# Kernel optimization log

Measured on AMD Instinct MI355X. Metric: run time of the kernel, lower is better.

## Reference

```python
import jax, jax.numpy as jnp
import numpy as np

B, H, S, D = 512, 1024, 1024, 128
TOPK = 32

def setup_inputs() -> dict:
    key = jax.random.key(0)
    ks = jax.random.split(key, 12)
    w = lambda k, shape: (jax.random.normal(k, shape, dtype=jnp.float32) * 0.02)
    return {
        "latent": jax.random.normal(ks[0], (B, H), dtype=jnp.float32),
        "memory": jax.random.normal(ks[1], (B, S, D), dtype=jnp.float32),
        "read_query_w": w(ks[2], (H, D)),
        "read_query_b": jnp.zeros((D,), jnp.float32),
        "memory_key": w(ks[3], (S, D)),
        "write_gate_w": w(ks[4], (H + D, 1)),
        "write_gate_b": jnp.zeros((1,), jnp.float32),
        "dmd_proj_w": w(ks[5], (H + D, 1)),
        "dmd_proj_b": jnp.zeros((1,), jnp.float32),
        "phase_proj_w": w(ks[6], (H, 1)),
        "phase_proj_b": jnp.zeros((1,), jnp.float32),
        "write_value_w": w(ks[7], (H, D)),
        "write_value_b": jnp.zeros((D,), jnp.float32),
    }

def reference(latent, memory, read_query_w, read_query_b, memory_key,
              write_gate_w, write_gate_b, dmd_proj_w, dmd_proj_b,
              phase_proj_w, phase_proj_b, write_value_w, write_value_b):
    # soft read over memory slots
    query = latent @ read_query_w + read_query_b              # [B, D]
    logits = jnp.einsum('bd,sd->bs', query, memory_key)       # [B, S]
    weights = jax.nn.softmax(logits, axis=-1)
    # top-k masked renormalization (topk=32 < S)
    _, topk_idx = jax.lax.top_k(weights, TOPK)                # [B, K]
    rows = jnp.arange(weights.shape[0])[:, None]
    mask = jnp.zeros_like(weights).at[rows, topk_idx].set(1.0)
    weights = weights * mask
    weights = weights / jnp.clip(weights.sum(-1, keepdims=True), 1e-8)
    read = jnp.einsum('bs,bsd->bd', weights, memory)          # [B, D]
    gate_input = jnp.concatenate([latent, read], axis=-1)     # [B, H+D]
    # sigmoid gate (gating_mode='sigmoid')
    gate = jax.nn.sigmoid(gate_input @ write_gate_w + write_gate_b)  # [B, 1]
    # dmd gating
    dmd_signal = jnp.tanh(gate_input @ dmd_proj_w + dmd_proj_b)
    gate = jnp.clip(gate * (0.75 + 0.5 * (dmd_signal + 1.0) * 0.5), 0.0, 1.0)
    # phase gating
    phase = latent @ phase_proj_w + phase_proj_b
    gate = gate * (0.5 * (1.0 + jnp.cos(phase)))
    # soft scatter-write update
    value = (latent @ write_value_w + write_value_b)[:, None, :]      # [B, 1, D]
    gw = gate[:, :, None] * weights[:, :, None]                       # [B, S, 1]
    new_memory = (1.0 - gw) * memory + gw * value                     # [B, S, D]
    return read, new_memory, weights
```

## Files before the change

kernel.cpp:

```cpp
#include <hip/hip_runtime.h>
#include <math.h>

#define NB 512
#define NH 1024
#define NS 1024
#define ND 128
#define NK 32

typedef float fx4 __attribute__((ext_vector_type(4)));

__global__ __launch_bounds__(512) void compute_kernel(
    const float* __restrict__ latent,
    const float* __restrict__ memory,
    const float* __restrict__ rq_w,
    const float* __restrict__ rq_b,
    const float* __restrict__ mem_key,
    const float* __restrict__ wg_w,
    const float* __restrict__ wg_b,
    const float* __restrict__ dmd_w,
    const float* __restrict__ dmd_b,
    const float* __restrict__ ph_w,
    const float* __restrict__ ph_b,
    const float* __restrict__ wv_w,
    const float* __restrict__ wv_b,
    float* __restrict__ out_read,
    float* __restrict__ out_wts,
    float* __restrict__ gw_out,
    float* __restrict__ valw)
{
  const int b    = blockIdx.x;
  const int tid  = threadIdx.x;
  const int lane = tid & 63;
  const int wv   = tid >> 6;

  __shared__ float lat[NH];
  __shared__ float wfull[NS];
  __shared__ float part[512];
  __shared__ float qv[ND];
  __shared__ float rd[ND];
  __shared__ float tvw[256];
  __shared__ int   tiw[256];
  __shared__ float wkL[NK];
  __shared__ int   tiL[NK];
  __shared__ float gred[24];
  __shared__ float scal[2];

  lat[tid]       = latent[(size_t)b * NH + tid];
  lat[tid + 512] = latent[(size_t)b * NH + tid + 512];
  __syncthreads();

  {
    const int d = tid & 127, p = tid >> 7;
    const float* W = rq_w + (size_t)(p * 256) * ND + d;
    const float* L = lat + p * 256;
    float acc = 0.f;
    #pragma unroll 8
    for (int h = 0; h < 256; ++h) acc = fmaf(L[h], W[(size_t)h * ND], acc);
    part[tid] = acc;
  }
  __syncthreads();
  if (tid < ND)
    qv[tid] = part[tid] + part[tid + 128] + part[tid + 256] + part[tid + 384] + rq_b[tid];
  __syncthreads();

  float r0 = 0.f, r1 = 0.f;
  {
    const float4* q4 = (const float4*)qv;
    const float4* k0 = (const float4*)(mem_key + (size_t)tid * ND);
    const float4* k1 = (const float4*)(mem_key + (size_t)(tid + 512) * ND);
    #pragma unroll 8
    for (int i = 0; i < ND / 4; ++i) {
      float4 q = q4[i];
      float4 x = k0[i];
      float4 y = k1[i];
      r0 += q.x * x.x + q.y * x.y + q.z * x.z + q.w * x.w;
      r1 += q.x * y.x + q.y * y.y + q.z * y.z + q.w * y.w;
    }
  }

  const float NEGINF = -3.0e38f;
  {
    const int s0 = tid, s1 = tid + 512;
    float v0 = r0, v1 = r1;
    for (int kk = 0; kk < NK; ++kk) {
      float best; int bi;
      if (v0 >= v1) { best = v0; bi = s0; } else { best = v1; bi = s1; }
      #pragma unroll
      for (int off = 1; off < 64; off <<= 1) {
        float ov = __shfl_xor(best, off);
        int   oi = __shfl_xor(bi, off);
        if (ov > best || (ov == best && oi < bi)) { best = ov; bi = oi; }
      }
      if (lane == 0) { tvw[(wv << 5) + kk] = best; tiw[(wv << 5) + kk] = bi; }
      if (bi == s0) v0 = NEGINF;
      if (bi == s1) v1 = NEGINF;
    }
  }
  wfull[tid] = 0.f; wfull[tid + 512] = 0.f;
  __syncthreads();

  float selv = NEGINF; int seli = -1; float wkreg = 0.f;
  if (wv == 0) {
    float m0 = tvw[lane], m1 = tvw[lane + 64], m2 = tvw[lane + 128], m3 = tvw[lane + 192];
    int   i0 = tiw[lane], i1 = tiw[lane + 64], i2 = tiw[lane + 128], i3 = tiw[lane + 192];
    for (int kk = 0; kk < NK; ++kk) {
      float best = m0; int bi = i0;
      if (m1 > best || (m1 == best && i1 < bi)) { best = m1; bi = i1; }
      if (m2 > best || (m2 == best && i2 < bi)) { best = m2; bi = i2; }
      if (m3 > best || (m3 == best && i3 < bi)) { best = m3; bi = i3; }
      #pragma unroll
      for (int off = 1; off < 64; off <<= 1) {
        float ov = __shfl_xor(best, off);
        int   oi = __shfl_xor(bi, off);
        if (ov > best || (ov == best && oi < bi)) { best = ov; bi = oi; }
      }
      if (kk == lane) { selv = best; seli = bi; }
      if (bi == i0) m0 = NEGINF;
      if (bi == i1) m1 = NEGINF;
      if (bi == i2) m2 = NEGINF;
      if (bi == i3) m3 = NEGINF;
    }
    float maxv = __shfl(selv, 0);
    float e = (lane < NK) ? expf(selv - maxv) : 0.f;
    float s = e;
    #pragma unroll
    for (int off = 1; off < 64; off <<= 1) s += __shfl_xor(s, off);
    wkreg = e / s;
    if (lane < NK) { wkL[lane] = wkreg; tiL[lane] = seli; }
  }
  __syncthreads();

  if (wv == 0 && lane < NK) wfull[seli] = wkreg;
  {
    const int d = tid & 127, p = tid >> 7;
    const float* mb = memory + (size_t)b * NS * ND;
    float racc = 0.f;
    #pragma unroll
    for (int k = p * 8; k < p * 8 + 8; ++k)
      racc = fmaf(wkL[k], mb[(size_t)tiL[k] * ND + d], racc);
    part[tid] = racc;
  }
  __syncthreads();
  if (tid < ND) {
    float r = part[tid] + part[tid + 128] + part[tid + 256] + part[tid + 384];
    rd[tid] = r;
    out_read[(size_t)b * ND + tid] = r;
  }
  __syncthreads();

  {
    float l0 = lat[tid], l1 = lat[tid + 512];
    float p1 = l0 * wg_w[tid]  + l1 * wg_w[tid + 512];
    float p2 = l0 * dmd_w[tid] + l1 * dmd_w[tid + 512];
    float p3 = l0 * ph_w[tid]  + l1 * ph_w[tid + 512];
    if (tid < ND) {
      float r = rd[tid];
      p1 += r * wg_w[NH + tid];
      p2 += r * dmd_w[NH + tid];
    }
    #pragma unroll
    for (int off = 1; off < 64; off <<= 1) {
      p1 += __shfl_xor(p1, off);
      p2 += __shfl_xor(p2, off);
      p3 += __shfl_xor(p3, off);
    }
    if (lane == 0) { gred[wv] = p1; gred[8 + wv] = p2; gred[16 + wv] = p3; }
  }
  {
    const int d = tid & 127, p = tid >> 7;
    const float* W = wv_w + (size_t)(p * 256) * ND + d;
    const float* L = lat + p * 256;
    float acc = 0.f;
    #pragma unroll 8
    for (int h = 0; h < 256; ++h) acc = fmaf(L[h], W[(size_t)h * ND], acc);
    part[tid] = acc;
  }
  __syncthreads();

  if (tid == 0) {
    float z1 = wg_b[0], z2 = dmd_b[0], z3 = ph_b[0];
    #pragma unroll
    for (int k = 0; k < 8; ++k) { z1 += gred[k]; z2 += gred[8 + k]; z3 += gred[16 + k]; }
    float g  = 1.f / (1.f + expf(-z1));
    float dm = tanhf(z2);
    g = g * (0.75f + 0.25f * (dm + 1.f));
    g = fminf(fmaxf(g, 0.f), 1.f);
    g = g * (0.5f * (1.f + cosf(z3)));
    scal[0] = g;
  }
  __syncthreads();

  {
    const float g = scal[0];
    float w0 = wfull[tid], w1 = wfull[tid + 512];
    out_wts[(size_t)b * NS + tid]       = w0;
    out_wts[(size_t)b * NS + tid + 512] = w1;
    gw_out [(size_t)b * NS + tid]       = g * w0;
    gw_out [(size_t)b * NS + tid + 512] = g * w1;
    if (tid < ND)
      valw[(size_t)b * ND + tid] =
          part[tid] + part[tid + 128] + part[tid + 256] + part[tid + 384] + wv_b[tid];
  }
}

__global__ __launch_bounds__(256) void copy_blend_kernel(
    const float* __restrict__ memory,
    const float* __restrict__ gw,
    const float* __restrict__ valw,
    float* __restrict__ out_mem)
{
  const size_t t = (size_t)blockIdx.x * 256 + threadIdx.x;
  const size_t stride = (size_t)8192 * 256;
  #pragma unroll
  for (int j = 0; j < 8; ++j) {
    size_t i = t + (size_t)j * stride;
    fx4 m = __builtin_nontemporal_load((const fx4*)memory + i);
    int row = (int)(i >> 5);
    float wgt = gw[row];
    fx4 o = m;
    if (wgt != 0.f) {
      float omw = 1.f - wgt;
      const fx4 v = *((const fx4*)valw + (size_t)((row >> 10) << 5) + (i & 31));
      o = omw * m + wgt * v;
    }
    __builtin_nontemporal_store(o, (fx4*)out_mem + i);
  }
}

extern "C" void kernel_launch(void* const* d_in, const int* in_sizes, int n_in,
                              void* d_out, int out_size, void* d_ws, size_t ws_size,
                              hipStream_t stream) {
  const float* latent  = (const float*)d_in[0];
  const float* memory  = (const float*)d_in[1];
  const float* rq_w    = (const float*)d_in[2];
  const float* rq_b    = (const float*)d_in[3];
  const float* mem_key = (const float*)d_in[4];
  const float* wg_w    = (const float*)d_in[5];
  const float* wg_b    = (const float*)d_in[6];
  const float* dmd_w   = (const float*)d_in[7];
  const float* dmd_b   = (const float*)d_in[8];
  const float* ph_w    = (const float*)d_in[9];
  const float* ph_b    = (const float*)d_in[10];
  const float* wv_w    = (const float*)d_in[11];
  const float* wv_b    = (const float*)d_in[12];

  float* out_read = (float*)d_out;
  float* out_mem  = out_read + (size_t)NB * ND;
  float* out_wts  = out_mem + (size_t)NB * NS * ND;

  float* gw   = (float*)d_ws;
  float* valw = gw + (size_t)NB * NS;

  compute_kernel<<<NB, 512, 0, stream>>>(
      latent, memory, rq_w, rq_b, mem_key, wg_w, wg_b, dmd_w, dmd_b,
      ph_w, ph_b, wv_w, wv_b, out_read, out_wts, gw, valw);

  copy_blend_kernel<<<8192, 256, 0, stream>>>(memory, gw, valw, out_mem);
}
```

Before: 546.5 us.

## Fuse memory copy-blend into compute kernel and interleave copy chunks with compute phases

Merges the separate copy/blend kernel into the per-batch compute kernel. Each block streams its batch's memory slab to the output in chunks placed between compute phases, so the copy overlaps the latency-bound top-k and matvec work. Afterwards it rewrites only the 32 selected rows with the blended values, removing the gw/valw workspace round trip and the second launch. Risk: register pressure from the 8-entry buffer, and bandwidth limited by having only 512 blocks.

Measured after the change: 517.0 us. -5.4%, faster.

```diff
diff --git a/kernel.cpp b/kernel.cpp
--- a/kernel.cpp
+++ b/kernel.cpp
@@ -9,7 +9,7 @@
 
 typedef float fx4 __attribute__((ext_vector_type(4)));
 
-__global__ __launch_bounds__(512) void compute_kernel(
+__global__ __launch_bounds__(512, 4) void fused_kernel(
     const float* __restrict__ latent,
     const float* __restrict__ memory,
     const float* __restrict__ rq_w,
@@ -24,9 +24,8 @@
     const float* __restrict__ wv_w,
     const float* __restrict__ wv_b,
     float* __restrict__ out_read,
-    float* __restrict__ out_wts,
-    float* __restrict__ gw_out,
-    float* __restrict__ valw)
+    float* __restrict__ out_mem,
+    float* __restrict__ out_wts)
 {
   const int b    = blockIdx.x;
   const int tid  = threadIdx.x;
@@ -36,19 +35,36 @@
   __shared__ float lat[NH];
   __shared__ float wfull[NS];
   __shared__ float part[512];
-  __shared__ float qv[ND];
+  __shared__ __align__(16) float qv[ND];
   __shared__ float rd[ND];
   __shared__ float tvw[256];
   __shared__ int   tiw[256];
   __shared__ float wkL[NK];
   __shared__ int   tiL[NK];
+  __shared__ __align__(16) float valw_s[ND];
   __shared__ float gred[24];
-  __shared__ float scal[2];
-
+  __shared__ float scal[1];
+
+  const fx4* __restrict__ msrc = (const fx4*)memory + (size_t)b * (NS * ND / 4);
+  fx4*       __restrict__ mdst = (fx4*)out_mem      + (size_t)b * (NS * ND / 4);
+  fx4 buf[8];
+  int cur = 0;
+
+#define CK_LOAD(N)  { _Pragma("unroll") \
+    for (int j = 0; j < (N); ++j) \
+      buf[j] = __builtin_nontemporal_load(msrc + (size_t)(cur + j) * 512 + tid); }
+#define CK_STORE(N) { _Pragma("unroll") \
+    for (int j = 0; j < (N); ++j) \
+      __builtin_nontemporal_store(buf[j], mdst + (size_t)(cur + j) * 512 + tid); \
+    cur += (N); }
+
+  CK_LOAD(8);
   lat[tid]       = latent[(size_t)b * NH + tid];
   lat[tid + 512] = latent[(size_t)b * NH + tid + 512];
-  __syncthreads();
-
+  CK_STORE(8);
+  __syncthreads();
+
+  CK_LOAD(4);
   {
     const int d = tid & 127, p = tid >> 7;
     const float* W = rq_w + (size_t)(p * 256) * ND + d;
@@ -58,12 +74,17 @@
     for (int h = 0; h < 256; ++h) acc = fmaf(L[h], W[(size_t)h * ND], acc);
     part[tid] = acc;
   }
-  __syncthreads();
+  CK_STORE(4);
+  __syncthreads();
+
+  CK_LOAD(8);
   if (tid < ND)
     qv[tid] = part[tid] + part[tid + 128] + part[tid + 256] + part[tid + 384] + rq_b[tid];
+  CK_STORE(8);
   __syncthreads();
 
   float r0 = 0.f, r1 = 0.f;
+  CK_LOAD(4);
   {
     const float4* q4 = (const float4*)qv;
     const float4* k0 = (const float4*)(mem_key + (size_t)tid * ND);
@@ -77,8 +98,11 @@
       r1 += q.x * y.x + q.y * y.y + q.z * y.z + q.w * y.w;
     }
   }
+  CK_STORE(4);
 
   const float NEGINF = -3.0e38f;
+  float selv = NEGINF; int seli = -1; float wkreg = 0.f;
+  CK_LOAD(4);
   {
     const int s0 = tid, s1 = tid + 512;
     float v0 = r0, v1 = r1;
@@ -97,9 +121,10 @@
     }
   }
   wfull[tid] = 0.f; wfull[tid + 512] = 0.f;
-  __syncthreads();
-
-  float selv = NEGINF; int seli = -1; float wkreg = 0.f;
+  CK_STORE(4);
+  __syncthreads();
+
+  CK_LOAD(8);
   if (wv == 0) {
     float m0 = tvw[lane], m1 = tvw[lane + 64], m2 = tvw[lane + 128], m3 = tvw[lane + 192];
     int   i0 = tiw[lane], i1 = tiw[lane + 64], i2 = tiw[lane + 128], i3 = tiw[lane + 192];
@@ -128,9 +153,11 @@
     wkreg = e / s;
     if (lane < NK) { wkL[lane] = wkreg; tiL[lane] = seli; }
   }
+  CK_STORE(8);
   __syncthreads();
 
   if (wv == 0 && lane < NK) wfull[seli] = wkreg;
+  CK_LOAD(4);
   {
     const int d = tid & 127, p = tid >> 7;
     const float* mb = memory + (size_t)b * NS * ND;
@@ -140,14 +167,19 @@
       racc = fmaf(wkL[k], mb[(size_t)tiL[k] * ND + d], racc);
     part[tid] = racc;
   }
-  __syncthreads();
+  CK_STORE(4);
+  __syncthreads();
+
+  CK_LOAD(8);
   if (tid < ND) {
     float r = part[tid] + part[tid + 128] + part[tid + 256] + part[tid + 384];
     rd[tid] = r;
     out_read[(size_t)b * ND + tid] = r;
   }
-  __syncthreads();
-
+  CK_STORE(8);
+  __syncthreads();
+
+  CK_LOAD(4);
   {
     float l0 = lat[tid], l1 = lat[tid + 512];
     float p1 = l0 * wg_w[tid]  + l1 * wg_w[tid + 512];
@@ -175,8 +207,10 @@
     for (int h = 0; h < 256; ++h) acc = fmaf(L[h], W[(size_t)h * ND], acc);
     part[tid] = acc;
   }
-  __syncthreads();
-
+  CK_STORE(4);
+  __syncthreads();
+
+  CK_LOAD(6);
   if (tid == 0) {
     float z1 = wg_b[0], z2 = dmd_b[0], z3 = ph_b[0];
     #pragma unroll
@@ -188,43 +222,37 @@
     g = g * (0.5f * (1.f + cosf(z3)));
     scal[0] = g;
   }
-  __syncthreads();
-
-  {
-    const float g = scal[0];
+  CK_STORE(6);
+  __syncthreads();
+
+  CK_LOAD(6);
+  {
     float w0 = wfull[tid], w1 = wfull[tid + 512];
     out_wts[(size_t)b * NS + tid]       = w0;
     out_wts[(size_t)b * NS + tid + 512] = w1;
-    gw_out [(size_t)b * NS + tid]       = g * w0;
-    gw_out [(size_t)b * NS + tid + 512] = g * w1;
     if (tid < ND)
-      valw[(size_t)b * ND + tid] =
-          part[tid] + part[tid + 128] + part[tid + 256] + part[tid + 384] + wv_b[tid];
-  }
-}
-
-__global__ __launch_bounds__(256) void copy_blend_kernel(
-    const float* __restrict__ memory,
-    const float* __restrict__ gw,
-    const float* __restrict__ valw,
-    float* __restrict__ out_mem)
-{
-  const size_t t = (size_t)blockIdx.x * 256 + threadIdx.x;
-  const size_t stride = (size_t)8192 * 256;
-  #pragma unroll
-  for (int j = 0; j < 8; ++j) {
-    size_t i = t + (size_t)j * stride;
-    fx4 m = __builtin_nontemporal_load((const fx4*)memory + i);
-    int row = (int)(i >> 5);
-    float wgt = gw[row];
-    fx4 o = m;
-    if (wgt != 0.f) {
-      float omw = 1.f - wgt;
-      const fx4 v = *((const fx4*)valw + (size_t)((row >> 10) << 5) + (i & 31));
-      o = omw * m + wgt * v;
-    }
-    __builtin_nontemporal_store(o, (fx4*)out_mem + i);
-  }
+      valw_s[tid] = part[tid] + part[tid + 128] + part[tid + 256] + part[tid + 384] + wv_b[tid];
+  }
+  CK_STORE(6);
+  __syncthreads();
+
+  {
+    const float g = scal[0];
+    const fx4* v4 = (const fx4*)valw_s;
+    #pragma unroll
+    for (int u = 0; u < 2; ++u) {
+      const int idx = tid + u * 512;
+      const int k   = idx >> 5;
+      const int c   = idx & 31;
+      const float w = g * wkL[k];
+      const int row = tiL[k];
+      const fx4 m = msrc[(size_t)row * 32 + c];
+      __builtin_nontemporal_store((1.f - w) * m + w * v4[c],
+                                  mdst + (size_t)row * 32 + c);
+    }
+  }
+#undef CK_LOAD
+#undef CK_STORE
 }
 
 extern "C" void kernel_launch(void* const* d_in, const int* in_sizes, int n_in,
@@ -248,12 +276,7 @@
   float* out_mem  = out_read + (size_t)NB * ND;
   float* out_wts  = out_mem + (size_t)NB * NS * ND;
 
-  float* gw   = (float*)d_ws;
-  float* valw = gw + (size_t)NB * NS;
-
-  compute_kernel<<<NB, 512, 0, stream>>>(
+  fused_kernel<<<NB, 512, 0, stream>>>(
       latent, memory, rq_w, rq_b, mem_key, wg_w, wg_b, dmd_w, dmd_b,
-      ph_w, ph_b, wv_w, wv_b, out_read, out_wts, gw, valw);
-
-  copy_blend_kernel<<<8192, 256, 0, stream>>>(memory, gw, valw, out_mem);
+      ph_w, ph_b, wv_w, wv_b, out_read, out_mem, out_wts);
 }
```
